# Performance work log

Measured on AMD Instinct MI355X. Metric: run time of the kernel, lower is better.

## Reference

```python
import jax, jax.numpy as jnp
import numpy as np

THRESH = 0.7
MASK_WEIGHT = 0.7
IM_WEIGHT = 0.3
P = 2

B, C, H, W = 32, 8, 256, 256


def setup_inputs() -> dict:
    key = jax.random.key(0)
    k1, k2 = jax.random.split(key)
    output = jax.random.normal(k1, (B, C, H, W), dtype=jnp.float32)
    target = jax.random.uniform(k2, (B, C, H, W), dtype=jnp.float32)  # mask channel in [0,1] for BCE
    return {"output": output, "target": target}


def _bce_mean(p, t):
    # torch.nn.BCELoss clamps log terms at -100
    logp = jnp.clip(jnp.log(p), -100.0)
    log1mp = jnp.clip(jnp.log1p(-p), -100.0)
    return -jnp.mean(t * logp + (1.0 - t) * log1mp, axis=(0, 2, 3))  # mean over B,H,W -> [G]


def reference(output, target):
    b, c, h, w = output.shape
    g = c // 4
    out = output.reshape(b, g, 4, h, w)
    tar = target.reshape(b, g, 4, h, w)

    out_mask = jax.nn.sigmoid(out[:, :, 3])          # [B,G,H,W]
    tar_mask = tar[:, :, 3]
    mask_loss = _bce_mean(out_mask, tar_mask)        # [G]

    diff = out[:, :, :3] - jax.lax.stop_gradient(tar[:, :, :3])  # target_img.detach()
    if P == 2:
        diff_norm = jnp.sqrt(jnp.sum(diff * diff, axis=2))       # [B,G,H,W]
    else:
        diff_norm = jnp.sum(jnp.abs(diff) ** P, axis=2) ** (1.0 / P)

    masked = jnp.where(out_mask > THRESH, diff_norm, 0.0)        # [B,G,H,W]
    count = jnp.sum(masked != 0.0, axis=(2, 3)).astype(diff_norm.dtype)  # [B,G] nonzero count
    msum = jnp.sum(masked, axis=(2, 3))                          # [B,G]
    fallback = jnp.mean(diff_norm, axis=(2, 3))                  # [B,G]
    per_sample = jnp.where(count > 0, msum / jnp.maximum(count, 1.0), fallback)
    nocs_loss = jnp.mean(per_sample, axis=0)                     # [G] (sum over batch / batch_size)

    loss_per_group = MASK_WEIGHT * mask_loss + IM_WEIGHT * nocs_loss
    return jnp.mean(loss_per_group)  # TotalLoss / Den
```

## Files before the change

kernel.cpp:

```cpp
#include <hip/hip_runtime.h>

constexpr int   Bsz = 32, Csz = 8, Hsz = 256, Wsz = 256;
constexpr int   HW  = Hsz * Wsz;
constexpr int   G   = Csz / 4;
constexpr int   NBG = Bsz * G;
constexpr float MASK_WEIGHT = 0.7f;
constexpr float IM_WEIGHT   = 0.3f;
constexpr float XTHRESH = 0.8472978603872037f;

constexpr int BLK   = 256;
constexpr int ITERS = 2;
constexpr int PIX4_PER_BG   = HW / 4;
constexpr int BLOCKS_PER_BG = PIX4_PER_BG / (BLK * ITERS);
constexpr int NB = NBG * BLOCKS_PER_BG;

typedef float fvec4 __attribute__((ext_vector_type(4)));


__global__ __launch_bounds__(256) void lp_mask_main(
    const float* __restrict__ out, const float* __restrict__ tar,
    float* __restrict__ ws)
{
    const int tid   = threadIdx.x;
    const int blk   = blockIdx.x;
    const int bg    = blk / BLOCKS_PER_BG;
    const int chunk = blk % BLOCKS_PER_BG;

    const size_t base = (size_t)bg * 4 * HW;
    const fvec4* po = reinterpret_cast<const fvec4*>(out + base);
    const fvec4* pt = reinterpret_cast<const fvec4*>(tar + base);
    constexpr int P4 = HW / 4;

    float bce = 0.0f, msum = 0.0f, cnt = 0.0f, dsum = 0.0f;

    constexpr float LOG2E = 1.4426950408889634f;
    constexpr float LN2   = 0.6931471805599453f;

#pragma unroll
    for (int it = 0; it < ITERS; ++it) {
        const int idx = chunk * (BLK * ITERS) + it * BLK + tid;
        const fvec4 a0 = __builtin_nontemporal_load(&po[idx]);
        const fvec4 a1 = __builtin_nontemporal_load(&po[idx + P4]);
        const fvec4 a2 = __builtin_nontemporal_load(&po[idx + 2 * P4]);
        const fvec4 a3 = __builtin_nontemporal_load(&po[idx + 3 * P4]);
        const fvec4 b0 = __builtin_nontemporal_load(&pt[idx]);
        const fvec4 b1 = __builtin_nontemporal_load(&pt[idx + P4]);
        const fvec4 b2 = __builtin_nontemporal_load(&pt[idx + 2 * P4]);
        const fvec4 b3 = __builtin_nontemporal_load(&pt[idx + 3 * P4]);

#pragma unroll
        for (int e = 0; e < 4; ++e) {
            const float x  = a3[e];
            const float t  = b3[e];
            const float d0 = a0[e] - b0[e];
            const float d1 = a1[e] - b1[e];
            const float d2 = a2[e] - b2[e];

            const float ax = __builtin_fabsf(x);
            const float ex = __builtin_exp2f(-ax * LOG2E);
            const float sp = fmaxf(x, 0.0f) + __builtin_log2f(1.0f + ex) * LN2;
            bce += __builtin_fmaf(t, x, -sp);

            const float dn = __builtin_sqrtf(d0 * d0 + d1 * d1 + d2 * d2);
            dsum += dn;
            if (x > XTHRESH) {
                msum += dn;
                cnt  += (dn != 0.0f) ? 1.0f : 0.0f;
            }
        }
    }

#pragma unroll
    for (int off = 32; off > 0; off >>= 1) {
        bce  += __shfl_down(bce,  off, 64);
        msum += __shfl_down(msum, off, 64);
        cnt  += __shfl_down(cnt,  off, 64);
        dsum += __shfl_down(dsum, off, 64);
    }

    __shared__ float s[4][4];
    const int wave = tid >> 6, lane = tid & 63;
    if (lane == 0) {
        s[wave][0] = bce; s[wave][1] = msum; s[wave][2] = cnt; s[wave][3] = dsum;
    }
    __syncthreads();
    if (tid == 0) {
        float rb = 0.0f, rm = 0.0f, rc = 0.0f, rd = 0.0f;
#pragma unroll
        for (int w = 0; w < 4; ++w) {
            rb += s[w][0]; rm += s[w][1]; rc += s[w][2]; rd += s[w][3];
        }
        ws[blk]          = rb;
        ws[NB + blk]     = rm;
        ws[2 * NB + blk] = rc;
        ws[3 * NB + blk] = rd;
    }
}

__global__ __launch_bounds__(64) void lp_mask_final(
    const float* __restrict__ ws, float* __restrict__ outp)
{
    const int t = threadIdx.x;
    constexpr int NPB = BLOCKS_PER_BG;
    const fvec4* wb = reinterpret_cast<const fvec4*>(ws) + t * (NPB / 4);
    const fvec4* wm = reinterpret_cast<const fvec4*>(ws + NB) + t * (NPB / 4);
    const fvec4* wc = reinterpret_cast<const fvec4*>(ws + 2 * NB) + t * (NPB / 4);
    const fvec4* wd = reinterpret_cast<const fvec4*>(ws + 3 * NB) + t * (NPB / 4);

    float b = 0.0f, m = 0.0f, c = 0.0f, d = 0.0f;
#pragma unroll
    for (int i = 0; i < NPB / 4; ++i) {
        const fvec4 vb = wb[i], vm = wm[i], vc = wc[i], vd = wd[i];
        b += vb[0] + vb[1] + vb[2] + vb[3];
        m += vm[0] + vm[1] + vm[2] + vm[3];
        c += vc[0] + vc[1] + vc[2] + vc[3];
        d += vd[0] + vd[1] + vd[2] + vd[3];
    }

    float ps = (c > 0.0f) ? (m / fmaxf(c, 1.0f)) : (d / (float)HW);

#pragma unroll
    for (int off = 32; off > 0; off >>= 1) {
        ps += __shfl_down(ps, off, 64);
        b  += __shfl_down(b,  off, 64);
    }

    if (t == 0) {
        const float mask_mean = -b / ((float)G * (float)Bsz * (float)HW);
        const float nocs_mean = ps / (float)(Bsz * G);
        outp[0] = MASK_WEIGHT * mask_mean + IM_WEIGHT * nocs_mean;
    }
}

extern "C" void kernel_launch(void* const* d_in, const int* in_sizes, int n_in,
                              void* d_out, int out_size, void* d_ws, size_t ws_size,
                              hipStream_t stream) {
    const float* out = (const float*)d_in[0];
    const float* tar = (const float*)d_in[1];
    float* ws = (float*)d_ws;
    float* o  = (float*)d_out;

    lp_mask_main<<<NB, BLK, 0, stream>>>(out, tar, ws);
    lp_mask_final<<<1, 64, 0, stream>>>(ws, o);
}
```

Measured before the change: 139.6 us.

## Double-buffer input loads through LDS with direct global-to-LDS async copies

Replaces the direct nontemporal vector loads with global_load_lds copies into a two-stage LDS buffer. The next iteration's tile is issued before the current one is consumed, and manual vmcnt waits overlap memory latency with compute. ITERS is doubled to give the pipeline more stages. In exchange each block now needs 64 KB of dynamic LDS, which limits how many blocks fit per CU, and correctness depends on the hand-coded waitcnt encoding.

```diff
diff --git a/kernel.cpp b/kernel.cpp
--- a/kernel.cpp
+++ b/kernel.cpp
@@ -9,13 +9,15 @@
 constexpr float XTHRESH = 0.8472978603872037f;
 
 constexpr int BLK   = 256;
-constexpr int ITERS = 2;
+constexpr int ITERS = 4;
 constexpr int PIX4_PER_BG   = HW / 4;
 constexpr int BLOCKS_PER_BG = PIX4_PER_BG / (BLK * ITERS);
 constexpr int NB = NBG * BLOCKS_PER_BG;
 
 typedef float fvec4 __attribute__((ext_vector_type(4)));
 
+
+#define WAITCNT_VM(n) __builtin_amdgcn_s_waitcnt(0x0F70 | ((n) & 0xF) | (((n) >> 4) << 14))
 
 __global__ __launch_bounds__(256) void lp_mask_main(
     const float* __restrict__ out, const float* __restrict__ tar,
@@ -31,22 +33,52 @@
     const fvec4* pt = reinterpret_cast<const fvec4*>(tar + base);
     constexpr int P4 = HW / 4;
 
+    extern __shared__ fvec4 lds[];
+
+    const int lbase = (tid >> 6) * 64;
+    const int idx0  = chunk * (BLK * ITERS) + tid;
+
+    auto stage = [&](int buf, int it) {
+        const int idx = idx0 + it * BLK;
+#pragma unroll
+        for (int p = 0; p < 4; ++p)
+            __builtin_amdgcn_global_load_lds(
+                (const __attribute__((address_space(1))) void*)&po[idx + p * P4],
+                (__attribute__((address_space(3))) void*)&lds[(buf * 8 + p) * 256 + lbase],
+                16, 0, 0);
+#pragma unroll
+        for (int p = 0; p < 4; ++p)
+            __builtin_amdgcn_global_load_lds(
+                (const __attribute__((address_space(1))) void*)&pt[idx + p * P4],
+                (__attribute__((address_space(3))) void*)&lds[((buf * 8 + 4 + p) * 256) + lbase],
+                16, 0, 0);
+    };
+
     float bce = 0.0f, msum = 0.0f, cnt = 0.0f, dsum = 0.0f;
-
     constexpr float LOG2E = 1.4426950408889634f;
     constexpr float LN2   = 0.6931471805599453f;
 
+    stage(0, 0);
+
 #pragma unroll
     for (int it = 0; it < ITERS; ++it) {
-        const int idx = chunk * (BLK * ITERS) + it * BLK + tid;
-        const fvec4 a0 = __builtin_nontemporal_load(&po[idx]);
-        const fvec4 a1 = __builtin_nontemporal_load(&po[idx + P4]);
-        const fvec4 a2 = __builtin_nontemporal_load(&po[idx + 2 * P4]);
-        const fvec4 a3 = __builtin_nontemporal_load(&po[idx + 3 * P4]);
-        const fvec4 b0 = __builtin_nontemporal_load(&pt[idx]);
-        const fvec4 b1 = __builtin_nontemporal_load(&pt[idx + P4]);
-        const fvec4 b2 = __builtin_nontemporal_load(&pt[idx + 2 * P4]);
-        const fvec4 b3 = __builtin_nontemporal_load(&pt[idx + 3 * P4]);
+        const int buf = it & 1;
+        if (it + 1 < ITERS) {
+            stage(buf ^ 1, it + 1);
+            WAITCNT_VM(8);
+        } else {
+            WAITCNT_VM(0);
+        }
+        asm volatile("" ::: "memory");
+
+        const fvec4 a0 = lds[(buf * 8 + 0) * 256 + tid];
+        const fvec4 a1 = lds[(buf * 8 + 1) * 256 + tid];
+        const fvec4 a2 = lds[(buf * 8 + 2) * 256 + tid];
+        const fvec4 a3 = lds[(buf * 8 + 3) * 256 + tid];
+        const fvec4 b0 = lds[(buf * 8 + 4) * 256 + tid];
+        const fvec4 b1 = lds[(buf * 8 + 5) * 256 + tid];
+        const fvec4 b2 = lds[(buf * 8 + 6) * 256 + tid];
+        const fvec4 b3 = lds[(buf * 8 + 7) * 256 + tid];
 
 #pragma unroll
         for (int e = 0; e < 4; ++e) {
@@ -68,6 +100,7 @@
                 cnt  += (dn != 0.0f) ? 1.0f : 0.0f;
             }
         }
+        asm volatile("" ::: "memory");
     }
 
 #pragma unroll
@@ -140,6 +173,6 @@
     float* ws = (float*)d_ws;
     float* o  = (float*)d_out;
 
-    lp_mask_main<<<NB, BLK, 0, stream>>>(out, tar, ws);
+    lp_mask_main<<<NB, BLK, 65536, stream>>>(out, tar, ws);
     lp_mask_final<<<1, 64, 0, stream>>>(ws, o);
 }
```

After: 143.1 us. 2.5% more time.
